# Performance work log

Measured on AMD Instinct MI355X. Metric: run time of the kernel, lower is better.

Reference implementation:

```python
import jax, jax.numpy as jnp
import numpy as np

DOF = 7
B = 8192
DT = 0.1
ACTION_RANGE = 50.0
MAX_VEL = 20.0


def _skew(w):
    x, y, z = w[..., 0], w[..., 1], w[..., 2]
    O = jnp.zeros_like(x)
    return jnp.stack([jnp.stack([O, -z, y], -1),
                      jnp.stack([z, O, -x], -1),
                      jnp.stack([-y, x, O], -1)], -2)


def _exp_se3(xi):
    # xi: (..., 6) twist [w; v] (already scaled by joint angle) -> (..., 4, 4)
    w, v = xi[..., :3], xi[..., 3:]
    th = jnp.sqrt(jnp.sum(w * w, -1))
    small = th < 1e-4
    ths = jnp.where(small, 1.0, th)  # safe denominator
    th2 = th * th
    a = jnp.where(small, 1.0 - th2 / 6.0, jnp.sin(th) / ths)
    b = jnp.where(small, 0.5 - th2 / 24.0, (1.0 - jnp.cos(th)) / (ths * ths))
    c = jnp.where(small, 1.0 / 6.0 - th2 / 120.0, (th - jnp.sin(th)) / (ths * ths * ths))
    K = _skew(w)
    K2 = K @ K
    I3 = jnp.eye(3, dtype=xi.dtype)
    R = I3 + a[..., None, None] * K + b[..., None, None] * K2
    Vm = I3 + b[..., None, None] * K + c[..., None, None] * K2
    p = jnp.einsum('...ij,...j->...i', Vm, v)
    top = jnp.concatenate([R, p[..., None]], -1)
    bot = jnp.broadcast_to(jnp.array([0.0, 0.0, 0.0, 1.0], xi.dtype), top.shape[:-2] + (1, 4))
    return jnp.concatenate([top, bot], -2)


def _inv_T(T):
    R = T[..., :3, :3]
    p = T[..., :3, 3]
    Rt = jnp.swapaxes(R, -1, -2)
    pn = -jnp.einsum('...ij,...j->...i', Rt, p)
    top = jnp.concatenate([Rt, pn[..., None]], -1)
    bot = jnp.broadcast_to(jnp.array([0.0, 0.0, 0.0, 1.0], T.dtype), top.shape[:-2] + (1, 4))
    return jnp.concatenate([top, bot], -2)


def _adjoint(T):
    # SE(3) adjoint for [w; v] twists: [[R, 0], [ [p]x R, R ]]
    R = T[..., :3, :3]
    p = T[..., :3, 3]
    pR = _skew(p) @ R
    Z = jnp.zeros_like(R)
    return jnp.concatenate([jnp.concatenate([R, Z], -1),
                            jnp.concatenate([pR, R], -1)], -2)


def _ad(V):
    # se(3) little adjoint: [[ [w]x, 0 ], [ [v]x, [w]x ]]
    Kw = _skew(V[..., :3])
    Kv = _skew(V[..., 3:])
    Z = jnp.zeros_like(Kw)
    return jnp.concatenate([jnp.concatenate([Kw, Z], -1),
                            jnp.concatenate([Kv, Kw], -1)], -2)


def _inverse_dynamics(q, dq, ddq, g, Ftip, M, G, A):
    # Recursive Newton-Euler (Modern Robotics, link-frame screws A).
    Bq, n = q.shape
    V = jnp.zeros((Bq, 6), q.dtype)
    Vd = jnp.broadcast_to(jnp.concatenate([jnp.zeros(3, q.dtype), -g]), (Bq, 6))
    AdTs, Vs, Vds = [], [], []
    for i in range(n):
        T = _exp_se3(-A[i] * q[:, i, None]) @ _inv_T(M[i])  # T_{i,i-1}, (B,4,4)
        AdT = _adjoint(T)
        V = jnp.einsum('bij,bj->bi', AdT, V) + A[i] * dq[:, i, None]
        Vd = (jnp.einsum('bij,bj->bi', AdT, Vd)
              + jnp.einsum('bij,j->bi', _ad(V), A[i]) * dq[:, i, None]
              + A[i] * ddq[:, i, None])
        AdTs.append(AdT)
        Vs.append(V)
        Vds.append(Vd)
    F = jnp.broadcast_to(Ftip.astype(q.dtype), (Bq, 6))
    AdT_end = _adjoint(_inv_T(M[n]))  # T_{n+1,n}, (6,6)
    taus = [None] * n
    for i in range(n - 1, -1, -1):
        if i == n - 1:
            F = jnp.einsum('ji,bj->bi', AdT_end, F)
        else:
            F = jnp.einsum('bji,bj->bi', AdTs[i + 1], F)
        F = (F + jnp.einsum('ij,bj->bi', G[i], Vds[i])
             - jnp.einsum('bji,jk,bk->bi', _ad(Vs[i]), G[i], Vs[i]))
        taus[i] = jnp.einsum('bi,i->b', F, A[i])
    return jnp.stack(taus, -1)  # (B, n)


def _forward_dynamics(q, dq, tau, g, Ftip, M, G, A):
    n = q.shape[1]
    zer = jnp.zeros_like(q)
    # bias forces: Coriolis + gravity + end-effector wrench
    h = _inverse_dynamics(q, dq, zer, g, Ftip, M, G, A)
    g0 = jnp.zeros(3, q.dtype)
    f0 = jnp.zeros(6, q.dtype)
    # mass matrix columns via unit accelerations (vmapped over columns)
    cols = jax.vmap(lambda e: _inverse_dynamics(
        q, zer, jnp.broadcast_to(e, q.shape), g0, f0, M, G, A))(jnp.eye(n, dtype=q.dtype))
    Mmat = jnp.transpose(cols, (1, 2, 0))  # (B, n, n)
    return jnp.linalg.solve(Mmat, (tau - h)[..., None])[..., 0]


def _fk_in_space(q, M, A):
    Bq, n = q.shape
    T = jnp.broadcast_to(jnp.eye(4, dtype=q.dtype), (Bq, 4, 4))
    outs = []
    for i in range(n):
        T = (T @ M[i]) @ _exp_se3(A[i] * q[:, i, None])
        outs.append(T)
    outs.append(T @ M[n])
    return jnp.stack(outs, 1)  # (B, n+1, 4, 4)


def setup_inputs():
    key = jax.random.key(0)
    ks = jax.random.split(key, 4)
    state = jax.random.normal(ks[0], (B, 2 * DOF), jnp.float32)
    torque = jax.random.normal(ks[1], (B, DOF), jnp.float32)
    M = jnp.tile(jnp.eye(4, dtype=jnp.float32)[None], (DOF + 1, 1, 1))
    A = jax.random.uniform(ks[2], (DOF, 6), jnp.float32)
    L = jax.random.normal(ks[3], (DOF, 6, 6), jnp.float32)
    gravity = jnp.array([0.0, -9.8, 0.0], jnp.float32)
    ftip = jnp.zeros(6, jnp.float32)
    return {"state": state, "torque": torque, "M": M, "A": A, "L": L,
            "gravity": gravity, "ftip": ftip}


def reference(state, torque, M, A, L, gravity, ftip):
    n = DOF
    G = L @ jnp.swapaxes(L, -1, -2)  # spatial inertias, PSD
    s0 = jnp.concatenate([state, torque * ACTION_RANGE], -1)  # (B, 3n)

    def derivs(s):
        q = s[..., :n]
        dq = s[..., n:2 * n]
        qf = s[..., 2 * n:]
        qacc = _forward_dynamics(q, dq, qf, gravity, ftip, M, G, A)
        return jnp.concatenate([dq, qacc, jnp.zeros_like(qf)], -1)

    k1 = derivs(s0)
    k2 = derivs(s0 + 0.5 * DT * k1)
    k3 = derivs(s0 + 0.5 * DT * k2)
    k4 = derivs(s0 + DT * k3)
    s1 = s0 + (DT / 6.0) * (k1 + 2.0 * k2 + 2.0 * k3 + k4)
    q = jnp.mod(s1[..., :n] + jnp.pi, 2.0 * jnp.pi) - jnp.pi
    dq = jnp.clip(s1[..., n:2 * n], -MAX_VEL, MAX_VEL)
    ee = _fk_in_space(q, M, A)
    return jnp.concatenate([q, dq], -1), ee[:, -1, :2, 3]
```

## Files before the change

kernel.cpp:

```cpp
#include <hip/hip_runtime.h>
#include <hip/hip_bf16.h>

#define DTC 0.1f
#define ACTION_RANGE 50.0f
#define MAX_VEL 20.0f
#define PI_F 3.14159265358979323846f
#define TWO_PI_F 6.28318530717958647692f
#define INV_TWO_PI_F 0.15915494309189533577f

__device__ __forceinline__ float bf2f(__hip_bfloat16 x){ return __bfloat162float(x); }
__device__ __forceinline__ float frcp(float x){ return __builtin_amdgcn_rcpf(x); }

__device__ __forceinline__ float ldv(const void* p, int i, bool isb){
  return isb ? __bfloat162float(((const __hip_bfloat16*)p)[i]) : ((const float*)p)[i];
}
__device__ __forceinline__ void stv(void* p, int i, float v, bool isb){
  if (isb) ((__hip_bfloat16*)p)[i] = __float2bfloat16(v);
  else     ((float*)p)[i] = v;
}

__device__ __forceinline__ void exp_se3_Rp(const float* Aj, float s, float* R, float* P){
  float wx=Aj[0]*s, wy=Aj[1]*s, wz=Aj[2]*s;
  float vx=Aj[3]*s, vy=Aj[4]*s, vz=Aj[5]*s;
  float th2 = wx*wx+wy*wy+wz*wz;
  float th = sqrtf(th2);
  float th4 = th2*th2;
  float aS = 1.f - th2*(1.f/6.f)  + th4*(1.f/120.f);
  float bS = 0.5f - th2*(1.f/24.f) + th4*(1.f/720.f);
  float cS = (1.f/6.f) - th2*(1.f/120.f) + th4*(1.f/5040.f);
  float sn = __sinf(th), cs = __cosf(th);
  float inv = frcp(th), inv2 = inv*inv;
  float aL = sn*inv;
  float bL = (1.f-cs)*inv2;
  float cL = (th-sn)*inv2*inv;
  bool sm = th < 0.25f;
  float a = sm?aS:aL, b = sm?bS:bL, c = sm?cS:cL;
  R[0]=1.f+b*(wx*wx-th2); R[1]=b*wx*wy-a*wz;      R[2]=b*wx*wz+a*wy;
  R[3]=b*wx*wy+a*wz;      R[4]=1.f+b*(wy*wy-th2); R[5]=b*wy*wz-a*wx;
  R[6]=b*wx*wz-a*wy;      R[7]=b*wy*wz+a*wx;      R[8]=1.f+b*(wz*wz-th2);
  float V0=1.f+c*(wx*wx-th2), V1=c*wx*wy-b*wz,      V2=c*wx*wz+b*wy;
  float V3=c*wx*wy+b*wz,      V4=1.f+c*(wy*wy-th2), V5=c*wy*wz-b*wx;
  float V6=c*wx*wz-b*wy,      V7=c*wy*wz+b*wx,      V8=1.f+c*(wz*wz-th2);
  P[0]=V0*vx+V1*vy+V2*vz;
  P[1]=V3*vx+V4*vy+V5*vz;
  P[2]=V6*vx+V7*vy+V8*vz;
}

__device__ __forceinline__ void mul33(const float* X, const float* Y, float* Z){
  #pragma unroll
  for (int r=0;r<3;r++){
    float x0=X[r*3+0], x1=X[r*3+1], x2=X[r*3+2];
    Z[r*3+0]=x0*Y[0]+x1*Y[3]+x2*Y[6];
    Z[r*3+1]=x0*Y[1]+x1*Y[4]+x2*Y[7];
    Z[r*3+2]=x0*Y[2]+x1*Y[5]+x2*Y[8];
  }
}

__device__ __forceinline__ void ad_apply(const float* R, const float* p, const float* Vin, float* Vout){
  float i0=Vin[0],i1=Vin[1],i2=Vin[2],i3=Vin[3],i4=Vin[4],i5=Vin[5];
  float w0 = R[0]*i0+R[1]*i1+R[2]*i2;
  float w1 = R[3]*i0+R[4]*i1+R[5]*i2;
  float w2 = R[6]*i0+R[7]*i1+R[8]*i2;
  float r0 = R[0]*i3+R[1]*i4+R[2]*i5;
  float r1 = R[3]*i3+R[4]*i4+R[5]*i5;
  float r2 = R[6]*i3+R[7]*i4+R[8]*i5;
  float p0=p[0],p1=p[1],p2=p[2];
  Vout[0]=w0; Vout[1]=w1; Vout[2]=w2;
  Vout[3]=p1*w2-p2*w1+r0;
  Vout[4]=p2*w0-p0*w2+r1;
  Vout[5]=p0*w1-p1*w0+r2;
}

__device__ __forceinline__ void adT_apply(const float* R, const float* p, const float* Fin, float* Fout){
  float m0=Fin[0],m1=Fin[1],m2=Fin[2],f0=Fin[3],f1=Fin[4],f2=Fin[5];
  float p0=p[0],p1=p[1],p2=p[2];
  float cx = m0 - (p1*f2 - p2*f1);
  float cy = m1 - (p2*f0 - p0*f2);
  float cz = m2 - (p0*f1 - p1*f0);
  float o0 = R[0]*cx + R[3]*cy + R[6]*cz;
  float o1 = R[1]*cx + R[4]*cy + R[7]*cz;
  float o2 = R[2]*cx + R[5]*cy + R[8]*cz;
  float o3 = R[0]*f0 + R[3]*f1 + R[6]*f2;
  float o4 = R[1]*f0 + R[4]*f1 + R[7]*f2;
  float o5 = R[2]*f0 + R[5]*f1 + R[8]*f2;
  Fout[0]=o0;Fout[1]=o1;Fout[2]=o2;Fout[3]=o3;Fout[4]=o4;Fout[5]=o5;
}

__device__ __forceinline__ void gmatvec(const float* G, const float* v, float* out){
  float v0=v[0],v1=v[1],v2=v[2],v3=v[3],v4=v[4],v5=v[5];
  #pragma unroll
  for (int r=0;r<6;r++)
    out[r] = G[r*6+0]*v0+G[r*6+1]*v1+G[r*6+2]*v2+G[r*6+3]*v3+G[r*6+4]*v4+G[r*6+5]*v5;
}

#define W_STRIDE 100

__global__ __launch_bounds__(64) void arm_rk4_kernel(
    const void* __restrict__ g_state,
    const void* __restrict__ g_torque,
    const void* __restrict__ g_M,
    const void* __restrict__ g_A,
    const void* __restrict__ g_L,
    const void* __restrict__ g_grav,
    const void* __restrict__ g_ftip,
    void* __restrict__ g_out,
    int B)
{
  __shared__ float sA[42];
  __shared__ float sG[252];
  __shared__ float sMinvR[72];
  __shared__ float sMinvp[24];
  __shared__ float sMR[72];
  __shared__ float sMp[24];
  __shared__ float sgrav[3];
  __shared__ float sftip[6];
  __shared__ float sW[8*W_STRIDE];

  const bool isb = fabsf(bf2f(((const __hip_bfloat16*)g_grav)[1]) + 9.8f) < 0.5f;

  const int t = threadIdx.x;
  for (int x=t; x<42; x+=64) sA[x] = ldv(g_A, x, isb);
  for (int x=t; x<252; x+=64){
    int i = x/36; int rc = x - i*36; int rr = rc/6; int cc = rc - rr*6;
    float s = 0.f;
    #pragma unroll
    for (int k=0;k<6;k++) s += ldv(g_L, i*36+rr*6+k, isb) * ldv(g_L, i*36+cc*6+k, isb);
    sG[x] = s;
  }
  if (t < 8){
    float R[9], p[3];
    #pragma unroll
    for (int rr=0;rr<3;rr++){
      #pragma unroll
      for (int cc=0;cc<3;cc++) R[rr*3+cc] = ldv(g_M, t*16 + rr*4 + cc, isb);
      p[rr] = ldv(g_M, t*16 + rr*4 + 3, isb);
    }
    #pragma unroll
    for (int rr=0;rr<3;rr++){
      #pragma unroll
      for (int cc=0;cc<3;cc++){ sMR[t*9+rr*3+cc] = R[rr*3+cc]; sMinvR[t*9+rr*3+cc] = R[cc*3+rr]; }
      sMp[t*3+rr] = p[rr];
      sMinvp[t*3+rr] = -(R[0*3+rr]*p[0] + R[1*3+rr]*p[1] + R[2*3+rr]*p[2]);
    }
  }
  if (t == 0){ for (int k=0;k<3;k++) sgrav[k] = ldv(g_grav, k, isb); }
  if (t == 1){ for (int k=0;k<6;k++) sftip[k] = ldv(g_ftip, k, isb); }
  __syncthreads();

  const int e = t >> 3;
  const int r = t & 7;
  int b = blockIdx.x * 8 + e;
  if (b >= B) b = B - 1;
  const bool is7 = (r == 7);
  float* W = &sW[e*W_STRIDE];

  float q0[7], dq0[7], qf[7];
  #pragma unroll
  for (int i=0;i<7;i++){
    q0[i]  = ldv(g_state, b*14+i, isb);
    dq0[i] = ldv(g_state, b*14+7+i, isb);
    qf[i]  = ldv(g_torque, b*7+i, isb) * ACTION_RANGE;
  }
  float kq[7], kdd[7], accq[7], accdq[7];
  #pragma unroll
  for (int i=0;i<7;i++){ kq[i]=0.f; kdd[i]=0.f; accq[i]=0.f; accdq[i]=0.f; }

  float Fend[6];
  {
    float tf[6]; adT_apply(&sMinvR[63], &sMinvp[21], sftip, tf);
    #pragma unroll
    for (int k=0;k<6;k++) Fend[k] = is7 ? tf[k] : 0.f;
  }

  #pragma unroll 1
  for (int st=0; st<4; ++st){
    const float cin = (st==0) ? 0.f : ((st==3) ? DTC : 0.5f*DTC);
    const float wgt = (st==0||st==3) ? (DTC/6.f) : (DTC/3.f);
    float qs[7], dqs[7];
    #pragma unroll
    for (int i=0;i<7;i++){ qs[i]=q0[i]+cin*kq[i]; dqs[i]=dq0[i]+cin*kdd[i]; }

    float qsr = 0.f;
    #pragma unroll
    for (int c=0;c<7;c++) qsr = (r==c) ? qs[c] : qsr;

    if (r < 7){
      float Re[9], Pe[3], Rt[9];
      exp_se3_Rp(&sA[r*6], -qsr, Re, Pe);
      mul33(Re, &sMinvR[r*9], Rt);
      float Tw[12];
      #pragma unroll
      for (int k=0;k<9;k++) Tw[k] = Rt[k];
      #pragma unroll
      for (int rr=0;rr<3;rr++)
        Tw[9+rr] = Re[rr*3+0]*sMinvp[r*3+0] + Re[rr*3+1]*sMinvp[r*3+1]
                 + Re[rr*3+2]*sMinvp[r*3+2] + Pe[rr];
      #pragma unroll
      for (int k=0;k<12;k++) W[r*12+k] = Tw[k];
    }
    __syncthreads();

    float Va[7][6], Vda[7][6];
    float V[6] = {0,0,0,0,0,0};
    float Vd[6];
    Vd[0]=0.f; Vd[1]=0.f; Vd[2]=0.f;
    Vd[3] = is7 ? -sgrav[0] : 0.f;
    Vd[4] = is7 ? -sgrav[1] : 0.f;
    Vd[5] = is7 ? -sgrav[2] : 0.f;
    #pragma unroll
    for (int i=0;i<7;i++){
      float Tl[12];
      #pragma unroll
      for (int k=0;k<12;k++) Tl[k] = W[i*12+k];
      const float* R = Tl;
      const float* p = Tl+9;
      float dqi  = is7 ? dqs[i] : 0.f;
      float ddqi = is7 ? 0.f : ((r==i) ? 1.f : 0.f);
      ad_apply(R,p,V,V);
      #pragma unroll
      for (int k=0;k<6;k++) V[k] += sA[i*6+k]*dqi;
      ad_apply(R,p,Vd,Vd);
      {
        float w0=V[0],w1=V[1],w2=V[2],v0=V[3],v1=V[4],v2=V[5];
        float a0=sA[i*6+0],a1=sA[i*6+1],a2=sA[i*6+2],a3=sA[i*6+3],a4=sA[i*6+4],a5=sA[i*6+5];
        Vd[0] += (w1*a2-w2*a1)*dqi + a0*ddqi;
        Vd[1] += (w2*a0-w0*a2)*dqi + a1*ddqi;
        Vd[2] += (w0*a1-w1*a0)*dqi + a2*ddqi;
        Vd[3] += ((v1*a2-v2*a1)+(w1*a5-w2*a4))*dqi + a3*ddqi;
        Vd[4] += ((v2*a0-v0*a2)+(w2*a3-w0*a5))*dqi + a4*ddqi;
        Vd[5] += ((v0*a1-v1*a0)+(w0*a4-w1*a3))*dqi + a5*ddqi;
      }
      #pragma unroll
      for (int k=0;k<6;k++){ Va[i][k]=V[k]; Vda[i][k]=Vd[k]; }
    }

    float m[7];
    {
      float F[6];
      #pragma unroll
      for (int k=0;k<6;k++) F[k] = Fend[k];
      #pragma unroll
      for (int i=6;i>=0;i--){
        if (i<6){
          float Tl[12];
          #pragma unroll
          for (int k=0;k<12;k++) Tl[k] = W[(i+1)*12+k];
          adT_apply(Tl, Tl+9, F, F);
        }
        float gv[6], gvd[6];
        gmatvec(&sG[i*36], Va[i], gv);
        gmatvec(&sG[i*36], Vda[i], gvd);
        float w0=Va[i][0],w1=Va[i][1],w2=Va[i][2],v0=Va[i][3],v1=Va[i][4],v2=Va[i][5];
        F[0] += gvd[0] + (w1*gv[2]-w2*gv[1]) + (v1*gv[5]-v2*gv[4]);
        F[1] += gvd[1] + (w2*gv[0]-w0*gv[2]) + (v2*gv[3]-v0*gv[5]);
        F[2] += gvd[2] + (w0*gv[1]-w1*gv[0]) + (v0*gv[4]-v1*gv[3]);
        F[3] += gvd[3] + (w1*gv[5]-w2*gv[4]);
        F[4] += gvd[4] + (w2*gv[3]-w0*gv[5]);
        F[5] += gvd[5] + (w0*gv[4]-w1*gv[3]);
        m[i] = F[0]*sA[i*6+0]+F[1]*sA[i*6+1]+F[2]*sA[i*6+2]
             + F[3]*sA[i*6+3]+F[4]*sA[i*6+4]+F[5]*sA[i*6+5];
      }
    }

    float rhs = 0.f;
    #pragma unroll
    for (int c=0;c<7;c++){
      float hc = __shfl(m[c], 7, 8);
      rhs = (r==c) ? (qf[c]-hc) : rhs;
    }
    #pragma unroll
    for (int k=0;k<7;k++){
      float pvk   = __shfl(m[k], k, 8);
      float pvrhs = __shfl(rhs,  k, 8);
      float pinv  = 1.f/pvk;
      float f = (r>k) ? m[k]*pinv : 0.f;
      #pragma unroll
      for (int c=k+1;c<7;c++){
        float pvc = __shfl(m[c], k, 8);
        m[c] -= f*pvc;
      }
      rhs -= f*pvrhs;
    }
    float x[7];
    #pragma unroll
    for (int i=6;i>=0;i--){
      float di = __shfl(m[i], i, 8);
      float si = __shfl(rhs, i, 8);
      float xi = si/di;
      x[i] = xi;
      rhs -= ((r<i) ? m[i] : 0.f) * xi;
    }

    #pragma unroll
    for (int i=0;i<7;i++){
      kq[i]  = dqs[i];
      kdd[i] = x[i];
      accq[i]  += wgt*dqs[i];
      accdq[i] += wgt*x[i];
    }
    __syncthreads();
  }

  float q1r=0.f, dq1r=0.f;
  #pragma unroll
  for (int c=0;c<7;c++){
    float xx = q0[c] + accq[c] + PI_F;
    float mm = xx - floorf(xx * INV_TWO_PI_F) * TWO_PI_F;
    float qv = mm - PI_F;
    float dv = dq0[c] + accdq[c];
    dv = fminf(fmaxf(dv, -MAX_VEL), MAX_VEL);
    q1r  = (r==c) ? qv : q1r;
    dq1r = (r==c) ? dv : dq1r;
  }

  {
    float XR[9], Xp[3];
    if (r < 7){
      float Re[9], Pe[3];
      exp_se3_Rp(&sA[r*6], q1r, Re, Pe);
      mul33(&sMR[r*9], Re, XR);
      #pragma unroll
      for (int rr=0;rr<3;rr++)
        Xp[rr] = sMR[r*9+rr*3+0]*Pe[0]+sMR[r*9+rr*3+1]*Pe[1]+sMR[r*9+rr*3+2]*Pe[2] + sMp[r*3+rr];
    } else {
      #pragma unroll
      for (int k=0;k<9;k++) XR[k] = sMR[63+k];
      #pragma unroll
      for (int k=0;k<3;k++) Xp[k] = sMp[21+k];
    }
    #pragma unroll
    for (int k=0;k<9;k++) W[r*12+k]   = XR[k];
    #pragma unroll
    for (int k=0;k<3;k++) W[r*12+9+k] = Xp[k];
  }
  __syncthreads();

  #pragma unroll
  for (int w=4; w>=1; w>>=1){
    float Ra[9], pa[3], Rb[9], pb[3];
    if (r < w){
      #pragma unroll
      for (int k=0;k<9;k++){ Ra[k]=W[(2*r)*12+k]; Rb[k]=W[(2*r+1)*12+k]; }
      #pragma unroll
      for (int k=0;k<3;k++){ pa[k]=W[(2*r)*12+9+k]; pb[k]=W[(2*r+1)*12+9+k]; }
    }
    __syncthreads();
    if (r < w){
      float Rc[9];
      mul33(Ra, Rb, Rc);
      #pragma unroll
      for (int k=0;k<9;k++) W[r*12+k] = Rc[k];
      #pragma unroll
      for (int rr=0;rr<3;rr++)
        W[r*12+9+rr] = Ra[rr*3+0]*pb[0]+Ra[rr*3+1]*pb[1]+Ra[rr*3+2]*pb[2] + pa[rr];
    }
    __syncthreads();
  }

  if (r < 7){
    stv(g_out, b*14+r,   q1r,  isb);
    stv(g_out, b*14+7+r, dq1r, isb);
  } else {
    stv(g_out, B*14 + b*2 + 0, W[9],  isb);
    stv(g_out, B*14 + b*2 + 1, W[10], isb);
  }
}

extern "C" void kernel_launch(void* const* d_in, const int* in_sizes, int n_in,
                              void* d_out, int out_size, void* d_ws, size_t ws_size,
                              hipStream_t stream) {
  const int B = in_sizes[0] / 14;
  const int blocks = (B + 7) / 8;
  arm_rk4_kernel<<<blocks, 64, 0, stream>>>(d_in[0], d_in[1], d_in[2], d_in[3],
                                            d_in[4], d_in[5], d_in[6], d_out, B);
}
```

Baseline: 93.62 us.

## Fold inertial force terms into forward pass and solve mass matrix redundantly per lane

The per-link G*V and Coriolis force terms are now computed during the forward velocity sweep and stored as six accumulated values per link, instead of keeping two 7x6 velocity arrays alive for the backward sweep. This cuts register pressure and the backward pass work. The distributed Gaussian elimination, which used many cross-lane shuffles with serialized pivots, is replaced by gathering the upper triangle of the symmetric mass matrix into every lane and solving it locally with an LDL-style elimination using fast reciprocals. This trades shuffle latency for redundant per-lane arithmetic and a 7x7 register array, and the fast reciprocal lowers precision slightly.

```diff
diff --git a/kernel.cpp b/kernel.cpp
--- a/kernel.cpp
+++ b/kernel.cpp
@@ -200,7 +200,7 @@
     }
     __syncthreads();
 
-    float Va[7][6], Vda[7][6];
+    float sacc[7][6];
     float V[6] = {0,0,0,0,0,0};
     float Vd[6];
     Vd[0]=0.f; Vd[1]=0.f; Vd[2]=0.f;
@@ -230,8 +230,18 @@
         Vd[4] += ((v2*a0-v0*a2)+(w2*a3-w0*a5))*dqi + a4*ddqi;
         Vd[5] += ((v0*a1-v1*a0)+(w0*a4-w1*a3))*dqi + a5*ddqi;
       }
-      #pragma unroll
-      for (int k=0;k<6;k++){ Va[i][k]=V[k]; Vda[i][k]=Vd[k]; }
+      float gv[6], gvd[6];
+      gmatvec(&sG[i*36], V, gv);
+      gmatvec(&sG[i*36], Vd, gvd);
+      {
+        float w0=V[0],w1=V[1],w2=V[2],v0=V[3],v1=V[4],v2=V[5];
+        sacc[i][0] = gvd[0] + (w1*gv[2]-w2*gv[1]) + (v1*gv[5]-v2*gv[4]);
+        sacc[i][1] = gvd[1] + (w2*gv[0]-w0*gv[2]) + (v2*gv[3]-v0*gv[5]);
+        sacc[i][2] = gvd[2] + (w0*gv[1]-w1*gv[0]) + (v0*gv[4]-v1*gv[3]);
+        sacc[i][3] = gvd[3] + (w1*gv[5]-w2*gv[4]);
+        sacc[i][4] = gvd[4] + (w2*gv[3]-w0*gv[5]);
+        sacc[i][5] = gvd[5] + (w0*gv[4]-w1*gv[3]);
+      }
     }
 
     float m[7];
@@ -247,48 +257,40 @@
           for (int k=0;k<12;k++) Tl[k] = W[(i+1)*12+k];
           adT_apply(Tl, Tl+9, F, F);
         }
-        float gv[6], gvd[6];
-        gmatvec(&sG[i*36], Va[i], gv);
-        gmatvec(&sG[i*36], Vda[i], gvd);
-        float w0=Va[i][0],w1=Va[i][1],w2=Va[i][2],v0=Va[i][3],v1=Va[i][4],v2=Va[i][5];
-        F[0] += gvd[0] + (w1*gv[2]-w2*gv[1]) + (v1*gv[5]-v2*gv[4]);
-        F[1] += gvd[1] + (w2*gv[0]-w0*gv[2]) + (v2*gv[3]-v0*gv[5]);
-        F[2] += gvd[2] + (w0*gv[1]-w1*gv[0]) + (v0*gv[4]-v1*gv[3]);
-        F[3] += gvd[3] + (w1*gv[5]-w2*gv[4]);
-        F[4] += gvd[4] + (w2*gv[3]-w0*gv[5]);
-        F[5] += gvd[5] + (w0*gv[4]-w1*gv[3]);
+        #pragma unroll
+        for (int k=0;k<6;k++) F[k] += sacc[i][k];
         m[i] = F[0]*sA[i*6+0]+F[1]*sA[i*6+1]+F[2]*sA[i*6+2]
              + F[3]*sA[i*6+3]+F[4]*sA[i*6+4]+F[5]*sA[i*6+5];
       }
     }
 
-    float rhs = 0.f;
-    #pragma unroll
-    for (int c=0;c<7;c++){
-      float hc = __shfl(m[c], 7, 8);
-      rhs = (r==c) ? (qf[c]-hc) : rhs;
-    }
+    float U[7][7];
+    #pragma unroll
+    for (int i=0;i<7;i++){
+      #pragma unroll
+      for (int j=i;j<7;j++) U[i][j] = __shfl(m[j], i, 8);
+    }
+    float rv[7];
+    #pragma unroll
+    for (int i=0;i<7;i++) rv[i] = qf[i] - __shfl(m[i], 7, 8);
     #pragma unroll
     for (int k=0;k<7;k++){
-      float pvk   = __shfl(m[k], k, 8);
-      float pvrhs = __shfl(rhs,  k, 8);
-      float pinv  = 1.f/pvk;
-      float f = (r>k) ? m[k]*pinv : 0.f;
-      #pragma unroll
-      for (int c=k+1;c<7;c++){
-        float pvc = __shfl(m[c], k, 8);
-        m[c] -= f*pvc;
+      float dinv = frcp(U[k][k]);
+      #pragma unroll
+      for (int i=k+1;i<7;i++){
+        float f = U[k][i]*dinv;
+        #pragma unroll
+        for (int j=i;j<7;j++) U[i][j] -= f*U[k][j];
+        rv[i] -= f*rv[k];
       }
-      rhs -= f*pvrhs;
     }
     float x[7];
     #pragma unroll
     for (int i=6;i>=0;i--){
-      float di = __shfl(m[i], i, 8);
-      float si = __shfl(rhs, i, 8);
-      float xi = si/di;
-      x[i] = xi;
-      rhs -= ((r<i) ? m[i] : 0.f) * xi;
+      float s = rv[i];
+      #pragma unroll
+      for (int j=i+1;j<7;j++) s -= U[i][j]*x[j];
+      x[i] = s*frcp(U[i][i]);
     }
 
     #pragma unroll
```

After: 101.2 us. 1.08x slower.
